# Optimization experiments

Hardware: AMD Instinct MI355X
Metric: run time of the kernel (lower is better)

The kernel has to match this reference:

```python
import jax, jax.numpy as jnp
import numpy as np

N, E, F, H, D, C = 50000, 800000, 128, 8, 16, 40


def setup_inputs() -> dict:
    key = jax.random.key(0)
    ks = jax.random.split(key, 12)
    s_in = 1.0 / np.sqrt(F)
    s_h = 1.0 / np.sqrt(H * D)
    return {
        "x": jax.random.normal(ks[0], (N, F), jnp.float32),
        "edge_index": jax.random.randint(ks[1], (2, E), 0, N, jnp.int64),
        "W1": jax.random.normal(ks[2], (F, H * D), jnp.float32) * s_in,
        "a_src1": jax.random.normal(ks[3], (H, D), jnp.float32) * s_h,
        "a_dst1": jax.random.normal(ks[4], (H, D), jnp.float32) * s_h,
        "b1": jnp.zeros((H * D,), jnp.float32),
        "W2": jax.random.normal(ks[5], (H * D, H * D), jnp.float32) * s_h,
        "a_src2": jax.random.normal(ks[6], (H, D), jnp.float32) * s_h,
        "a_dst2": jax.random.normal(ks[7], (H, D), jnp.float32) * s_h,
        "b2": jnp.zeros((H * D,), jnp.float32),
        "Wc": jax.random.normal(ks[8], (H * D, C), jnp.float32) * s_h,
        "bc": jnp.zeros((C,), jnp.float32),
    }


def _gat_layer(x, src, dst, W, a_src, a_dst, b):
    # x: [N, F_in]; src/dst: [E'] (self-loops already appended)
    n = x.shape[0]
    h, d = a_src.shape
    hx = (x @ W).reshape(n, h, d)                      # [N, H, D]
    al_src = jnp.einsum("nhd,hd->nh", hx, a_src)       # [N, H]
    al_dst = jnp.einsum("nhd,hd->nh", hx, a_dst)       # [N, H]
    e = jax.nn.leaky_relu(al_src[src] + al_dst[dst], 0.2)  # [E', H]
    # segment softmax over incoming edges of each destination node
    m = jax.ops.segment_max(e, dst, num_segments=n)    # [N, H]
    e = jnp.exp(e - m[dst])
    z = jax.ops.segment_sum(e, dst, num_segments=n)    # [N, H]
    alpha = e / z[dst]                                 # [E', H]
    out = jax.ops.segment_sum(alpha[:, :, None] * hx[src], dst, num_segments=n)
    return out.reshape(n, h * d) + b


def reference(x, edge_index, W1, a_src1, a_dst1, b1, W2, a_src2, a_dst2, b2, Wc, bc):
    n = x.shape[0]
    loops = jnp.arange(n, dtype=edge_index.dtype)
    src = jnp.concatenate([edge_index[0], loops])  # PyG GATConv adds self-loops
    dst = jnp.concatenate([edge_index[1], loops])
    h = _gat_layer(x, src, dst, W1, a_src1, a_dst1, b1)
    h = jax.nn.elu(h)  # ELU between layers (i < K-1); dropout=None -> no-op
    h = _gat_layer(h, src, dst, W2, a_src2, a_dst2, b2)
    return h @ Wc + bc  # [N, C] logits
```

## Files before the change

kernel.cpp:

```cpp
#include <hip/hip_runtime.h>
#include <hip/hip_bf16.h>
#include <hip/hip_fp16.h>


#define FDIM 128
#define HEADS 8

typedef short bf16x8 __attribute__((ext_vector_type(8)));
typedef float f32x4 __attribute__((ext_vector_type(4)));

__device__ __forceinline__ float leaky02(float x) {
    return fmaxf(x, 0.2f * x);
}

__device__ __forceinline__ unsigned pack2h(float x, float y) {
    __half2 h2 = __floats2half2_rn(x, y);
    return *(unsigned*)&h2;
}

__device__ __forceinline__ void split2(float x, unsigned short& hi, unsigned short& lo) {
    unsigned bits = __float_as_uint(x);
    unsigned h = bits + 0x7fffu + ((bits >> 16) & 1u);
    hi = (unsigned short)(h >> 16);
    float hf = __uint_as_float(h & 0xffff0000u);
    float r = x - hf;
    unsigned rb = __float_as_uint(r);
    unsigned l2 = rb + 0x7fffu + ((rb >> 16) & 1u);
    lo = (unsigned short)(l2 >> 16);
}


__global__ __launch_bounds__(256) void wconv_kernel(const float* __restrict__ W1,
                                                    const float* __restrict__ W2,
                                                    unsigned short* __restrict__ w1_hi,
                                                    unsigned short* __restrict__ w1_lo,
                                                    unsigned short* __restrict__ w2_hi,
                                                    unsigned short* __restrict__ w2_lo) {
    int b = blockIdx.x, t = threadIdx.x;
    const float* W = (b < 16) ? W1 : W2;
    unsigned short* whi = (b < 16) ? w1_hi : w2_hi;
    unsigned short* wlo = (b < 16) ? w1_lo : w2_lo;
    int idx = (b & 15) * 256 + t;
    int k = idx >> 5;
    int c0 = (idx & 31) * 4;
#pragma unroll
    for (int i = 0; i < 4; ++i) {
        int c = c0 + i;
        float v = W[k * FDIM + c];
        unsigned short h, l;
        split2(v, h, l);
        int dest = ((k >> 5) * 8 + (c >> 4)) * 512 +
                   ((c & 15) + (((k >> 3) & 3) << 4)) * 8 + (k & 7);
        whi[dest] = h;
        wlo[dest] = l;
    }
}


__global__ __launch_bounds__(256) void scan_partial(const int* __restrict__ deg,
                                                    int* __restrict__ partials,
                                                    int n) {
    __shared__ int red[256];
    int t = threadIdx.x;
    int base = blockIdx.x * 1024 + t * 4;
    int s = 0;
#pragma unroll
    for (int j = 0; j < 4; ++j) {
        int i = base + j;
        if (i < n) s += deg[i];
    }
    red[t] = s;
    __syncthreads();
    for (int off = 128; off > 0; off >>= 1) {
        if (t < off) red[t] += red[t + off];
        __syncthreads();
    }
    if (t == 0) partials[blockIdx.x] = red[0];
}

__global__ __launch_bounds__(256) void scan_final(const int* __restrict__ deg,
                                                  const int* __restrict__ partials,
                                                  int* __restrict__ row_start,
                                                  int n, int nb) {
    __shared__ int sbuf[256];
    __shared__ int boff_s, total_s;
    int t = threadIdx.x;
    if (t < 64) {
        int carry = 0;
        for (int base = 0; base < nb; base += 64) {
            int idx = base + t;
            int v = (idx < nb) ? partials[idx] : 0;
            int incl = v;
#pragma unroll
            for (int off = 1; off < 64; off <<= 1) {
                int x = __shfl_up(incl, off);
                if (t >= off) incl += x;
            }
            if (idx == (int)blockIdx.x) boff_s = carry + incl - v;
            carry += __shfl(incl, 63);
        }
        if (t == 0) total_s = carry;
    }
    __syncthreads();
    if (blockIdx.x == 0 && t == 0) row_start[n] = total_s;

    int base = blockIdx.x * 1024 + t * 4;
    int v[4];
#pragma unroll
    for (int j = 0; j < 4; ++j) v[j] = (base + j < n) ? deg[base + j] : 0;
    int tsum = v[0] + v[1] + v[2] + v[3];
    sbuf[t] = tsum;
    __syncthreads();
    for (int off = 1; off < 256; off <<= 1) {
        int tmp = (t >= off) ? sbuf[t - off] : 0;
        __syncthreads();
        sbuf[t] += tmp;
        __syncthreads();
    }
    int toff = boff_s + sbuf[t] - tsum;
    int run = 0;
#pragma unroll
    for (int j = 0; j < 4; ++j) {
        int i = base + j;
        if (i < n) row_start[i] = toff + run;
        run += v[j];
    }
}


__global__ __launch_bounds__(256) void scatter_kernel(const int* __restrict__ ei,
                                                      const int* __restrict__ rank,
                                                      const int* __restrict__ row_start,
                                                      int* __restrict__ csr_src,
                                                      int E) {
    int tid = threadIdx.x;
#pragma unroll
    for (int j = 0; j < 4; ++j) {
        int e = blockIdx.x * 1024 + j * 256 + tid;
        if (e < E) {
            int s = ei[e];
            int d = ei[E + e];
            __builtin_nontemporal_store(s, &csr_src[row_start[d] + rank[e]]);
        }
    }
}


template <bool FUSED>
__global__ __launch_bounds__(256, 3) void gemm_mfma(const float* __restrict__ xf,
                                                    const unsigned short* __restrict__ a_hi,
                                                    const unsigned short* __restrict__ a_lo,
                                                    const unsigned short* __restrict__ w_hi,
                                                    const unsigned short* __restrict__ w_lo,
                                                    const float* __restrict__ asrc,
                                                    const float* __restrict__ adst,
                                                    float* __restrict__ als,
                                                    float* __restrict__ ald,
                                                    unsigned* __restrict__ hxf,
                                                    int n,
                                                    const int* __restrict__ ei,
                                                    int* __restrict__ deg,
                                                    int* __restrict__ rank,
                                                    int E, int ng, int grid) {
    int tid = threadIdx.x;
    int gb;
    if (FUSED) {
        int bid = blockIdx.x;
        int t0 = (int)((long long)bid * ng / grid);
        int t1 = (int)((long long)(bid + 1) * ng / grid);
        if (t1 == t0) {
            int sb = bid - t0;
#pragma unroll
            for (int j = 0; j < 4; ++j) {
                int e = sb * 1024 + j * 256 + tid;
                if (e < E) rank[e] = atomicAdd(&deg[ei[E + e]], 1);
            }
            return;
        }
        gb = t0;
    } else {
        gb = blockIdx.x;
    }

    int lane = tid & 63;
    int wave = tid >> 6;
    int l15 = lane & 15;
    int lg = lane >> 4;
    int row0 = gb * 32;

    float4 xr[4][2][2];
    bf16x8 AH[4][2], AL[4][2];
#pragma unroll
    for (int kc = 0; kc < 4; ++kc) {
#pragma unroll
        for (int fr = 0; fr < 2; ++fr) {
            int r = row0 + fr * 16 + l15;
            if (r > n - 1) r = n - 1;
            if (FUSED) {
                const float* px = xf + (size_t)r * FDIM + kc * 32 + lg * 8;
                xr[kc][fr][0] = *(const float4*)px;
                xr[kc][fr][1] = *(const float4*)(px + 4);
            } else {
                size_t off = (size_t)r * FDIM + kc * 32 + lg * 8;
                AH[kc][fr] = *(const bf16x8*)(a_hi + off);
                AL[kc][fr] = *(const bf16x8*)(a_lo + off);
            }
        }
    }

    bf16x8 Bh[2][2], Bl[2][2];
#pragma unroll
    for (int fc = 0; fc < 2; ++fc) {
        size_t off = (size_t)(wave * 2 + fc) * 512 + lane * 8;
        Bh[0][fc] = *(const bf16x8*)(w_hi + off);
        Bl[0][fc] = *(const bf16x8*)(w_lo + off);
    }

    f32x4 acc[2][2];
#pragma unroll
    for (int fr = 0; fr < 2; ++fr)
#pragma unroll
        for (int fc = 0; fc < 2; ++fc)
#pragma unroll
            for (int r = 0; r < 4; ++r) acc[fr][fc][r] = 0.f;

#pragma unroll
    for (int kc = 0; kc < 4; ++kc) {
        const int cur = kc & 1, nxt = (kc & 1) ^ 1;
        if (kc < 3) {
#pragma unroll
            for (int fc = 0; fc < 2; ++fc) {
                size_t off = (size_t)((kc + 1) * 8 + wave * 2 + fc) * 512 + lane * 8;
                Bh[nxt][fc] = *(const bf16x8*)(w_hi + off);
                Bl[nxt][fc] = *(const bf16x8*)(w_lo + off);
            }
        }
        bf16x8 Ah[2], Al[2];
#pragma unroll
        for (int fr = 0; fr < 2; ++fr) {
            if (FUSED) {
                float vv[8] = {xr[kc][fr][0].x, xr[kc][fr][0].y,
                               xr[kc][fr][0].z, xr[kc][fr][0].w,
                               xr[kc][fr][1].x, xr[kc][fr][1].y,
                               xr[kc][fr][1].z, xr[kc][fr][1].w};
#pragma unroll
                for (int j = 0; j < 8; ++j) {
                    unsigned bits = __float_as_uint(vv[j]);
                    Ah[fr][j] = (short)(bits >> 16);
                    float hf = __uint_as_float(bits & 0xffff0000u);
                    Al[fr][j] = (short)(__float_as_uint(vv[j] - hf) >> 16);
                }
            } else {
                Ah[fr] = AH[kc][fr];
                Al[fr] = AL[kc][fr];
            }
        }
#pragma unroll
        for (int fr = 0; fr < 2; ++fr)
#pragma unroll
            for (int fc = 0; fc < 2; ++fc) {
                acc[fr][fc] = __builtin_amdgcn_mfma_f32_16x16x32_bf16(
                    Al[fr], Bh[cur][fc], acc[fr][fc], 0, 0, 0);
                acc[fr][fc] = __builtin_amdgcn_mfma_f32_16x16x32_bf16(
                    Ah[fr], Bl[cur][fc], acc[fr][fc], 0, 0, 0);
                acc[fr][fc] = __builtin_amdgcn_mfma_f32_16x16x32_bf16(
                    Ah[fr], Bh[cur][fc], acc[fr][fc], 0, 0, 0);
            }
    }

#pragma unroll
    for (int fr = 0; fr < 2; ++fr)
#pragma unroll
        for (int fc = 0; fc < 2; ++fc) {
            int CB = wave * 32 + fc * 16;
            int col = CB + l15;
            float as_ = asrc[col];
            float ad_ = adst[col];
#pragma unroll
            for (int reg = 0; reg < 4; ++reg) {
                int row = row0 + fr * 16 + lg * 4 + reg;
                float v = acc[fr][fc][reg];
                float vn = __shfl_xor(v, 1);
                if ((lane & 1) == 0 && row < n)
                    hxf[(size_t)row * 64 + (col >> 1)] = pack2h(v, vn);
                float ps = v * as_;
                float pd = v * ad_;
                ps += __shfl_xor(ps, 1);
                pd += __shfl_xor(pd, 1);
                ps += __shfl_xor(ps, 2);
                pd += __shfl_xor(pd, 2);
                ps += __shfl_xor(ps, 4);
                pd += __shfl_xor(pd, 4);
                ps += __shfl_xor(ps, 8);
                pd += __shfl_xor(pd, 8);
                if (l15 == 0 && row < n) {
                    als[row * HEADS + (CB >> 4)] = ps;
                    ald[row * HEADS + (CB >> 4)] = pd;
                }
            }
        }
}


__global__ __launch_bounds__(256, 8) void gemm_cls(const unsigned* __restrict__ h_f16,
                                                   const float* __restrict__ W,
                                                   const float* __restrict__ bias,
                                                   float* __restrict__ out,
                                                   int n) {
    __shared__ float xs[32][136];
    __shared__ float ws[32][48];
    int tid = threadIdx.x;
    int row0 = blockIdx.x * 128;
    int lane = tid & 63;
    int wave = tid >> 6;
    int lane2 = lane * 2;
    int wc = wave * 10;

    float acc[2][10];
#pragma unroll
    for (int i = 0; i < 2; ++i)
#pragma unroll
        for (int j = 0; j < 10; ++j) acc[i][j] = 0.f;

    for (int kc = 0; kc < 128; kc += 32) {
        if (kc) __syncthreads();
#pragma unroll
        for (int it = 0; it < 4; ++it) {
            int idx = it * 256 + tid;
            int r = idx >> 3, kg = (idx & 7) * 4;
            float4 v = make_float4(0.f, 0.f, 0.f, 0.f);
            if (row0 + r < n) {
                uint2 hh = *(const uint2*)&h_f16[(size_t)(row0 + r) * 64 + (kc + kg) / 2];
                float2 a = __half22float2(*(__half2*)&hh.x);
                float2 b = __half22float2(*(__half2*)&hh.y);
                v.x = a.x; v.y = a.y; v.z = b.x; v.w = b.y;
            }
            int col = r ^ kg;
            xs[kg + 0][col] = v.x;
            xs[kg + 1][col] = v.y;
            xs[kg + 2][col] = v.z;
            xs[kg + 3][col] = v.w;
        }
#pragma unroll
        for (int it = 0; it < 6; ++it) {
            int idx = it * 256 + tid;
            int kk = idx / 48, c = idx - kk * 48;
            ws[kk][c] = (c < 40) ? W[(size_t)(kc + kk) * 40 + c] : 0.f;
        }
        __syncthreads();
#pragma unroll
        for (int k = 0; k < 32; ++k) {
            int s = ((k >> 2) & 7) << 2;
            float2 av2 = *(const float2*)&xs[k][lane2 ^ s];
            float av[2] = {av2.x, av2.y};
#pragma unroll
            for (int j = 0; j < 10; ++j) {
                float w = ws[k][wc + j];
                acc[0][j] += av[0] * w;
                acc[1][j] += av[1] * w;
            }
        }
    }

#pragma unroll
    for (int i = 0; i < 2; ++i) {
        int row = row0 + lane2 + i;
        if (row < n) {
#pragma unroll
            for (int j = 0; j < 10; ++j)
                out[(size_t)row * 40 + wc + j] = acc[i][j] + bias[wc + j];
        }
    }
}


template <bool DOELU, bool WRITELO>
__global__ __launch_bounds__(256) void gat_aggregate(const unsigned* __restrict__ hxf,
                                                     const float* __restrict__ als,
                                                     const float* __restrict__ ald,
                                                     const int* __restrict__ row_start,
                                                     const int* __restrict__ csr_src,
                                                     const float* __restrict__ bias,
                                                     unsigned* __restrict__ h_hi,
                                                     unsigned* __restrict__ h_lo,
                                                     int n) {
    int wid = threadIdx.x >> 6;
    int lane = threadIdx.x & 63;
    int node = blockIdx.x * 4 + wid;
    if (node >= n) return;

    int rs = row_start[node];
    int deg = row_start[node + 1] - rs;

    int h = lane & 7;
    int hc = lane >> 3;
    int lq = lane >> 3;
    float ald_h = ald[node * HEADS + h];

    float acc0 = 0.f, acc1 = 0.f, zown = 0.f;
    int total = deg + 1;

    int ii = lq;
    int srcv = (ii < deg) ? csr_src[rs + ii] : node;
    float w = (ii < total) ? __expf(leaky02(als[srcv * HEADS + h] + ald_h)) : 0.f;

    int i0 = 0;
    for (; i0 + 8 <= total; i0 += 8) {
        zown += w;
        int ii_n = i0 + 8 + lq;
        int srcv_n = (ii_n < deg) ? csr_src[rs + ii_n] : node;
#pragma unroll
        for (int e = 0; e < 8; ++e) {
            int s = __builtin_amdgcn_readlane(srcv, e * 8);
            float we = __shfl(w, e * 8 + hc);
            unsigned v = hxf[(size_t)s * 64 + lane];
            float2 f = __half22float2(*(__half2*)&v);
            acc0 += we * f.x;
            acc1 += we * f.y;
        }
        float w_n = (ii_n < total) ? __expf(leaky02(als[srcv_n * HEADS + h] + ald_h)) : 0.f;
        srcv = srcv_n;
        w = w_n;
    }
    int rem = total - i0;
    if (rem > 0) {
        zown += w;
        for (int e = 0; e < rem; ++e) {
            int s = __builtin_amdgcn_readlane(srcv, e * 8);
            float we = __shfl(w, e * 8 + hc);
            unsigned v = hxf[(size_t)s * 64 + lane];
            float2 f = __half22float2(*(__half2*)&v);
            acc0 += we * f.x;
            acc1 += we * f.y;
        }
    }

    zown += __shfl_xor(zown, 8);
    zown += __shfl_xor(zown, 16);
    zown += __shfl_xor(zown, 32);
    float z = __shfl(zown, hc);

    float2 bv = *(const float2*)&bias[2 * lane];
    float o0 = acc0 / z + bv.x;
    float o1 = acc1 / z + bv.y;
    if (DOELU) {
        o0 = o0 > 0.f ? o0 : (__expf(o0) - 1.f);
        o1 = o1 > 0.f ? o1 : (__expf(o1) - 1.f);
    }
    if (WRITELO) {
        unsigned short hh0, ll0, hh1, ll1;
        split2(o0, hh0, ll0);
        split2(o1, hh1, ll1);
        h_hi[(size_t)node * 64 + lane] = (unsigned)hh0 | ((unsigned)hh1 << 16);
        h_lo[(size_t)node * 64 + lane] = (unsigned)ll0 | ((unsigned)ll1 << 16);
    } else {
        h_hi[(size_t)node * 64 + lane] = pack2h(o0, o1);
    }
}


extern "C" void kernel_launch(void* const* d_in, const int* in_sizes, int n_in,
                              void* d_out, int out_size, void* d_ws, size_t ws_size,
                              hipStream_t stream) {
    const float* x      = (const float*)d_in[0];
    const int*   ei     = (const int*)d_in[1];
    const float* W1     = (const float*)d_in[2];
    const float* a_src1 = (const float*)d_in[3];
    const float* a_dst1 = (const float*)d_in[4];
    const float* b1     = (const float*)d_in[5];
    const float* W2     = (const float*)d_in[6];
    const float* a_src2 = (const float*)d_in[7];
    const float* a_dst2 = (const float*)d_in[8];
    const float* b2     = (const float*)d_in[9];
    const float* Wc     = (const float*)d_in[10];
    const float* bc     = (const float*)d_in[11];
    float* out = (float*)d_out;

    const int N = in_sizes[0] / FDIM;
    const int E = in_sizes[1] / 2;
    const int NB = (N + 1023) / 1024;

    unsigned* hxf = (unsigned*)d_ws;
    unsigned* xh_u = hxf + (size_t)N * 64;
    unsigned* xl_u = xh_u + (size_t)N * 64;
    float* als  = (float*)(xl_u + (size_t)N * 64);
    float* ald  = als + (size_t)N * HEADS;
    unsigned short* w1_hi = (unsigned short*)(ald + (size_t)N * HEADS);
    unsigned short* w1_lo = w1_hi + 16384;
    unsigned short* w2_hi = w1_lo + 16384;
    unsigned short* w2_lo = w2_hi + 16384;
    int* deg       = (int*)(w2_lo + 16384);
    int* row_start = deg + N;
    int* partials  = row_start + ((N + 8) & ~3);
    int* rank      = partials + ((NB + 4) & ~3);
    int* csr_src   = rank + E;

    hipMemsetAsync(deg, 0, (size_t)N * sizeof(int), stream);
    wconv_kernel<<<32, 256, 0, stream>>>(W1, W2, w1_hi, w1_lo, w2_hi, w2_lo);

    const int ng = (N + 31) / 32;
    const int hb = (E + 1023) / 1024;
    const int grid1 = ng + hb;
    const int agg_grid = (N + 3) / 4;
    const int cls_grid = (N + 127) / 128;

    gemm_mfma<true><<<grid1, 256, 0, stream>>>(x, nullptr, nullptr,
                                               w1_hi, w1_lo,
                                               a_src1, a_dst1, als, ald, hxf, N,
                                               ei, deg, rank, E, ng, grid1);
    scan_partial<<<NB, 256, 0, stream>>>(deg, partials, N);
    scan_final<<<NB, 256, 0, stream>>>(deg, partials, row_start, N, NB);
    scatter_kernel<<<hb, 256, 0, stream>>>(ei, rank, row_start, csr_src, E);

    gat_aggregate<true, true><<<agg_grid, 256, 0, stream>>>(
        hxf, als, ald, row_start, csr_src, b1, xh_u, xl_u, N);
    gemm_mfma<false><<<ng, 256, 0, stream>>>(nullptr,
                                             (const unsigned short*)xh_u,
                                             (const unsigned short*)xl_u,
                                             w2_hi, w2_lo,
                                             a_src2, a_dst2, als, ald, hxf, N,
                                             nullptr, nullptr, nullptr, 0, ng, ng);
    gat_aggregate<false, false><<<agg_grid, 256, 0, stream>>>(
        hxf, als, ald, row_start, csr_src, b2, xh_u, xl_u, N);
    gemm_cls<<<cls_grid, 256, 0, stream>>>(xh_u, Wc, bc, out, N);
}
```

Before: 220.8 us.

## Stage GEMM A-tile through LDS with direct global-to-LDS loads and XOR swizzle

Instead of each lane loading its whole A-operand slice into registers up front, the block cooperatively copies the 32-row A tile into shared memory using global_load_lds with an XOR-swizzled layout, then reads fragments from LDS per k-chunk. This cuts register pressure, so launch bounds are raised to allow 4 blocks per CU. It adds a block barrier and 16KB of LDS per block, which may limit occupancy or add latency.

Measured after the change: 215.0 us. 2.6% less time.

```diff
diff --git a/kernel.cpp b/kernel.cpp
--- a/kernel.cpp
+++ b/kernel.cpp
@@ -8,6 +8,13 @@
 
 typedef short bf16x8 __attribute__((ext_vector_type(8)));
 typedef float f32x4 __attribute__((ext_vector_type(4)));
+
+typedef __attribute__((address_space(1))) const unsigned gu32;
+typedef __attribute__((address_space(3))) unsigned lu32;
+
+__device__ __forceinline__ void load_lds16(const void* g, void* l) {
+    __builtin_amdgcn_global_load_lds((gu32*)g, (lu32*)l, 16, 0, 0);
+}
 
 __device__ __forceinline__ float leaky02(float x) {
     return fmaxf(x, 0.2f * x);
@@ -147,7 +154,7 @@
 
 
 template <bool FUSED>
-__global__ __launch_bounds__(256, 3) void gemm_mfma(const float* __restrict__ xf,
+__global__ __launch_bounds__(256, 4) void gemm_mfma(const float* __restrict__ xf,
                                                     const unsigned short* __restrict__ a_hi,
                                                     const unsigned short* __restrict__ a_lo,
                                                     const unsigned short* __restrict__ w_hi,
@@ -162,6 +169,7 @@
                                                     int* __restrict__ deg,
                                                     int* __restrict__ rank,
                                                     int E, int ng, int grid) {
+    __shared__ __align__(16) char smem[16384];
     int tid = threadIdx.x;
     int gb;
     if (FUSED) {
@@ -188,23 +196,29 @@
     int lg = lane >> 4;
     int row0 = gb * 32;
 
-    float4 xr[4][2][2];
-    bf16x8 AH[4][2], AL[4][2];
-#pragma unroll
-    for (int kc = 0; kc < 4; ++kc) {
-#pragma unroll
-        for (int fr = 0; fr < 2; ++fr) {
-            int r = row0 + fr * 16 + l15;
-            if (r > n - 1) r = n - 1;
-            if (FUSED) {
-                const float* px = xf + (size_t)r * FDIM + kc * 32 + lg * 8;
-                xr[kc][fr][0] = *(const float4*)px;
-                xr[kc][fr][1] = *(const float4*)(px + 4);
-            } else {
-                size_t off = (size_t)r * FDIM + kc * 32 + lg * 8;
-                AH[kc][fr] = *(const bf16x8*)(a_hi + off);
-                AL[kc][fr] = *(const bf16x8*)(a_lo + off);
-            }
+    if (FUSED) {
+#pragma unroll
+        for (int c = 0; c < 4; ++c) {
+            int s = (wave * 4 + c) * 64 + lane;
+            int r = s >> 5, kkp = s & 31;
+            int kk = kkp ^ (r & 7);
+            int rg = row0 + r;
+            if (rg > n - 1) rg = n - 1;
+            load_lds16(xf + (size_t)rg * FDIM + kk * 4,
+                       smem + (size_t)(wave * 4 + c) * 1024);
+        }
+    } else {
+#pragma unroll
+        for (int c = 0; c < 2; ++c) {
+            int s = (wave * 2 + c) * 64 + lane;
+            int r = s >> 4, kkp = s & 15;
+            int kk = kkp ^ (r & 7);
+            int rg = row0 + r;
+            if (rg > n - 1) rg = n - 1;
+            load_lds16(a_hi + (size_t)rg * FDIM + kk * 8,
+                       smem + (size_t)(wave * 2 + c) * 1024);
+            load_lds16(a_lo + (size_t)rg * FDIM + kk * 8,
+                       smem + 8192 + (size_t)(wave * 2 + c) * 1024);
         }
     }
 
@@ -216,6 +230,8 @@
         Bl[0][fc] = *(const bf16x8*)(w_lo + off);
     }
 
+    __syncthreads();
+
     f32x4 acc[2][2];
 #pragma unroll
     for (int fr = 0; fr < 2; ++fr)
@@ -238,11 +254,12 @@
         bf16x8 Ah[2], Al[2];
 #pragma unroll
         for (int fr = 0; fr < 2; ++fr) {
+            int r = fr * 16 + l15;
             if (FUSED) {
-                float vv[8] = {xr[kc][fr][0].x, xr[kc][fr][0].y,
-                               xr[kc][fr][0].z, xr[kc][fr][0].w,
-                               xr[kc][fr][1].x, xr[kc][fr][1].y,
-                               xr[kc][fr][1].z, xr[kc][fr][1].w};
+                int kk0 = kc * 8 + lg * 2;
+                const float4 v0 = *(const float4*)(smem + r * 512 + ((kk0 ^ (r & 7)) << 4));
+                const float4 v1 = *(const float4*)(smem + r * 512 + (((kk0 + 1) ^ (r & 7)) << 4));
+                float vv[8] = {v0.x, v0.y, v0.z, v0.w, v1.x, v1.y, v1.z, v1.w};
 #pragma unroll
                 for (int j = 0; j < 8; ++j) {
                     unsigned bits = __float_as_uint(vv[j]);
@@ -251,8 +268,10 @@
                     Al[fr][j] = (short)(__float_as_uint(vv[j] - hf) >> 16);
                 }
             } else {
-                Ah[fr] = AH[kc][fr];
-                Al[fr] = AL[kc][fr];
+                int kk = kc * 4 + lg;
+                int off = r * 256 + ((kk ^ (r & 7)) << 4);
+                Ah[fr] = *(const bf16x8*)(smem + off);
+                Al[fr] = *(const bf16x8*)(smem + 8192 + off);
             }
         }
 #pragma unroll
```
